# Performance work log

Measured on AMD Instinct MI355X. Metric: run time of the kernel, lower is better.

Reference implementation:

```python
import jax, jax.numpy as jnp
import numpy as np

B, HH, WW, D, NH, DK, DV, RATIO = 16, 48, 48, 512, 8, 64, 64, 3
EPS = 1e-5

def setup_inputs() -> dict:
    key = jax.random.key(0)
    ks = jax.random.split(key, 12)
    nq = HH * WW
    w = lambda i, shape: jax.random.normal(ks[i], shape, jnp.float32) * 0.02
    return {
        "queries": jax.random.normal(ks[0], (B, nq, D), jnp.float32),
        "Wq": w(1, (D, NH * DK)), "bq": jnp.zeros((NH * DK,), jnp.float32),
        "Wk": w(2, (D, NH * DK)), "bk": jnp.zeros((NH * DK,), jnp.float32),
        "Wv": w(3, (D, NH * DV)), "bv": jnp.zeros((NH * DV,), jnp.float32),
        "Wo": w(4, (NH * DV, D)), "bo": jnp.zeros((D,), jnp.float32),
        "sr_w": w(5, (D, 1, RATIO + 1, RATIO + 1)),  # depthwise conv, OIHW with I=1
        "sr_b": jnp.zeros((D,), jnp.float32),
        "ln_g": jnp.ones((D,), jnp.float32), "ln_b": jnp.zeros((D,), jnp.float32),
        "tw": w(6, (NH, NH)),  # 1x1 conv over head dim
        "tb": jnp.zeros((NH,), jnp.float32),
    }


def reference(queries, Wq, bq, Wk, bk, Wv, bv, Wo, bo, sr_w, sr_b, ln_g, ln_b, tw, tb):
    b, nq, c = queries.shape
    # Q projection -> (b, h, nq, d_k)
    q = (queries @ Wq + bq).reshape(b, nq, NH, DK).transpose(0, 2, 1, 3)
    # spatial reduction: depthwise strided conv over (H, W)
    x = queries.transpose(0, 2, 1).reshape(b, c, HH, WW)
    pad = RATIO // 2
    x = jax.lax.conv_general_dilated(
        x, sr_w, window_strides=(RATIO, RATIO),
        padding=[(pad, pad), (pad, pad)], feature_group_count=c,
        dimension_numbers=("NCHW", "OIHW", "NCHW"))
    x = x + sr_b[None, :, None, None]
    nk = x.shape[2] * x.shape[3]
    x = x.reshape(b, c, nk).transpose(0, 2, 1)  # (b, nk, c)
    # LayerNorm over channel dim
    mu = x.mean(-1, keepdims=True)
    var = x.var(-1, keepdims=True)
    x = (x - mu) / jnp.sqrt(var + EPS) * ln_g + ln_b
    # K, V projections
    k = (x @ Wk + bk).reshape(b, nk, NH, DK).transpose(0, 2, 3, 1)  # (b,h,d_k,nk)
    v = (x @ Wv + bv).reshape(b, nk, NH, DV).transpose(0, 2, 1, 3)  # (b,h,nk,d_v)
    # scaled attention scores
    att = jnp.einsum("bhqd,bhdk->bhqk", q, k) / jnp.sqrt(jnp.float32(DK))
    # transform: 1x1 conv over heads -> softmax(-1) -> InstanceNorm2d (no affine)
    att = jnp.einsum("oi,biqk->boqk", tw, att) + tb[None, :, None, None]
    att = jax.nn.softmax(att, axis=-1)
    m = att.mean((2, 3), keepdims=True)
    va = att.var((2, 3), keepdims=True)
    att = (att - m) / jnp.sqrt(va + EPS)
    # apply to values and output projection
    out = jnp.einsum("bhqk,bhkd->bhqd", att, v).transpose(0, 2, 1, 3).reshape(b, nq, NH * DV)
    return out @ Wo + bo
```

## Files before the change

kernel.cpp:

```cpp
#include <hip/hip_runtime.h>
#include <hip/hip_bf16.h>
#include <stdint.h>


typedef __bf16 bf16;
typedef __bf16 bf16x4 __attribute__((ext_vector_type(4)));
typedef __bf16 bf16x8 __attribute__((ext_vector_type(8)));
typedef float  f32x4  __attribute__((ext_vector_type(4)));

#define LDS_AS  __attribute__((address_space(3)))
#define GLOB_AS __attribute__((address_space(1)))

__device__ __forceinline__ void gload_lds16(const bf16* g, void* l) {
    __builtin_amdgcn_global_load_lds((const GLOB_AS void*)g, (LDS_AS void*)l, 16, 0, 0);
}

#define NB   16
#define NQ   2304
#define DD   512
#define NKV  256

constexpr size_t OFF_WQT = 0;
constexpr size_t OFF_WKT = 512*512*2;
constexpr size_t OFF_WVT = 2*512*512*2;
constexpr size_t OFF_WOT = 3*512*512*2;
constexpr size_t OFF_X   = 4*512*512*2;
constexpr size_t OFF_KT  = OFF_X  + 4194304;
constexpr size_t OFF_VT  = OFF_KT + 4194304;
constexpr size_t OFF_SS  = OFF_VT + 4194304;
constexpr size_t OFF_SM  = OFF_SS + 512;
constexpr size_t OFF_TWF = OFF_SM + 40192;
constexpr size_t OFF_FLG = OFF_TWF + 256;
constexpr size_t OFF_QF  = OFF_FLG + 256;
constexpr size_t OFF_U   = OFF_QF + (size_t)NB*NQ*DD*2;
constexpr size_t OFF_S   = OFF_U  + (size_t)NB*NQ*DD*2;
constexpr size_t SPLANE  = (size_t)NQ*NKV*2;
constexpr size_t OFF_WOTP = OFF_X;

#define SM_BQ   0
#define SM_BK   512
#define SM_BV   1024
#define SM_BO   1536
#define SM_SRW  2048
#define SM_SRB  10240
#define SM_LNG  10752
#define SM_LNB  11264
#define SM_TW   11776
#define SM_SRWT 11840

__global__ __launch_bounds__(64) void detect_dtype(const uint32_t* __restrict__ q,
                                                   int* __restrict__ flag)
{
    int t = threadIdx.x;
    int cnt = 0;
    #pragma unroll
    for (int i = 0; i < 8; i++) {
        uint32_t w = q[t*8 + i];
        int e = (w >> 7) & 0xFF;
        cnt += (e >= 100 && e <= 150) ? 1 : 0;
    }
    #pragma unroll
    for (int m = 1; m < 64; m <<= 1) cnt += __shfl_xor(cnt, m);
    if (t == 0) *flag = (cnt >= 384) ? 0 : 1;
}

__global__ __launch_bounds__(256) void convert_q(const void* __restrict__ in,
                                                 bf16* __restrict__ out,
                                                 const int* __restrict__ flag)
{
    if (*flag == 0) return;
    int idx = blockIdx.x * 256 + threadIdx.x;
    f32x4 a = ((const f32x4*)in)[(size_t)idx*2];
    f32x4 b = ((const f32x4*)in)[(size_t)idx*2 + 1];
    bf16x8 r;
    #pragma unroll
    for (int i = 0; i < 4; i++) { r[i] = (bf16)a[i]; r[i+4] = (bf16)b[i]; }
    ((bf16x8*)out)[idx] = r;
}

__global__ __launch_bounds__(256) void convert_small(
    const void* s0, const void* s1, const void* s2, const void* s3,
    const void* s4, const void* s5, const void* s6, const void* s7,
    const void* s8, bf16* __restrict__ dst, float* __restrict__ twf,
    const int* __restrict__ flag)
{
    const void* srcs[9] = {s0,s1,s2,s3,s4,s5,s6,s7,s8};
    const int sizes[9]  = {512,512,512,512,8192,512,512,512,64};
    const int offs[9]   = {SM_BQ,SM_BK,SM_BV,SM_BO,SM_SRW,SM_SRB,SM_LNG,SM_LNB,SM_TW};
    const float scl[9]  = {0.125f,1.f,1.f,1.f,1.f,1.f,1.f,1.f,1.f};
    int b = blockIdx.x;
    const void* s = srcs[b];
    int n = sizes[b], o = offs[b];
    float sc = scl[b];
    bool f32 = (*flag != 0);
    for (int i = threadIdx.x; i < n; i += 256) {
        float v = f32 ? ((const float*)s)[i] : (float)((const bf16*)s)[i];
        dst[o + i] = (bf16)(v * sc);
        if (b == 8) twf[i] = v;
        if (b == 4) {
            int tap = i & 15, ch = i >> 4;
            dst[SM_SRWT + tap*DD + ch] = (bf16)v;
        }
    }
}

__global__ __launch_bounds__(256) void transpose512(
    const void* s0, const void* s1, const void* s2, const void* s3,
    bf16* __restrict__ d0, bf16* __restrict__ d1,
    bf16* __restrict__ d2, bf16* __restrict__ d3,
    const int* __restrict__ flag)
{
    __shared__ bf16 tile[32][33];
    bool f32 = (*flag != 0);
    int wsel = blockIdx.z;
    const void* src = wsel == 0 ? s0 : wsel == 1 ? s1 : wsel == 2 ? s2 : s3;
    bf16*       dst = wsel == 0 ? d0 : wsel == 1 ? d1 : wsel == 2 ? d2 : d3;
    float scl = (wsel == 0) ? 0.125f : 1.0f;
    int c0 = blockIdx.x * 32, n0 = blockIdx.y * 32;
    int tx = threadIdx.x, ty = threadIdx.y;
    #pragma unroll
    for (int i = 0; i < 4; i++) {
        size_t idx = (size_t)(c0 + ty + i*8) * 512 + n0 + tx;
        float v = f32 ? ((const float*)src)[idx] : (float)((const bf16*)src)[idx];
        tile[ty + i*8][tx] = (bf16)(v * scl);
    }
    __syncthreads();
    #pragma unroll
    for (int i = 0; i < 4; i++)
        dst[(size_t)(n0 + ty + i*8) * 512 + c0 + tx] = tile[tx][ty + i*8];
}

__global__ __launch_bounds__(256) void sr_ln(
    const void* __restrict__ qraw, const bf16* __restrict__ qc,
    const bf16* __restrict__ sm, bf16* __restrict__ x,
    const int* __restrict__ flag)
{
    const bf16* q = (*flag) ? qc : (const bf16*)qraw;
    const int t = threadIdx.x;
    const int w = t >> 6, lane = t & 63;
    const int pos = blockIdx.x * 4 + w;
    const int b = pos >> 8, ok = pos & 255;
    const int oh = ok >> 4, ow = ok & 15;
    const int c0 = lane * 8;

    float acc[8] = {};
    #pragma unroll
    for (int kh = 0; kh < 4; kh++) {
        int ih = oh*3 - 1 + kh;
        if (ih < 0) continue;
        #pragma unroll
        for (int kw = 0; kw < 4; kw++) {
            int iw = ow*3 - 1 + kw;
            if (iw < 0) continue;
            bf16x8 qv = *(const bf16x8*)(q + ((size_t)b*NQ + ih*48 + iw)*DD + c0);
            bf16x8 wv = *(const bf16x8*)(sm + SM_SRWT + (kh*4 + kw)*DD + c0);
            #pragma unroll
            for (int r = 0; r < 8; r++) acc[r] += (float)qv[r] * (float)wv[r];
        }
    }
    bf16x8 sb = *(const bf16x8*)(sm + SM_SRB + c0);
    #pragma unroll
    for (int r = 0; r < 8; r++) acc[r] += (float)sb[r];

    float s = 0.f, s2 = 0.f;
    #pragma unroll
    for (int r = 0; r < 8; r++) { s += acc[r]; s2 += acc[r]*acc[r]; }
    #pragma unroll
    for (int m = 1; m < 64; m <<= 1) { s += __shfl_xor(s, m); s2 += __shfl_xor(s2, m); }
    float mu  = s * (1.f/512.f);
    float var = s2 * (1.f/512.f) - mu*mu;
    float inv = rsqrtf(var + 1e-5f);

    bf16x8 gv = *(const bf16x8*)(sm + SM_LNG + c0);
    bf16x8 bv = *(const bf16x8*)(sm + SM_LNB + c0);
    bf16x8 outv;
    #pragma unroll
    for (int r = 0; r < 8; r++)
        outv[r] = (bf16)((acc[r] - mu) * inv * (float)gv[r] + (float)bv[r]);
    *(bf16x8*)(x + (size_t)pos * DD + c0) = outv;
}

template <int MODE>
__global__ __launch_bounds__(256) void gemm_bt(
    const bf16* __restrict__ A, const bf16* __restrict__ Bt,
    const bf16* __restrict__ bias, bf16* __restrict__ C,
    const int* __restrict__ of32, const bf16* __restrict__ A2)
{
    constexpr int K = 512;
    __shared__ bf16 Al[128 * 64];
    __shared__ bf16 Bl[128 * 64];
    const int m0 = blockIdx.x * 128, n0 = blockIdx.y * 128;
    const int t = threadIdx.x;
    const int lane = t & 63, w = t >> 6;
    const int wr = w >> 1, wc = w & 1;
    const int gg = lane >> 4, li = lane & 15;
    const int fsw = (li & 7) << 4;
    bool f32o = false;
    if (MODE == 2) f32o = (*of32 != 0);

    const bf16* Ab = A;
    if (MODE == 4) Ab = (*of32) ? A2 : A;
    const bf16* Btb = Bt;
    if (MODE == 2) Btb = Bt + (size_t)(m0 / 2304) * (512 * 512);

    f32x4 acc[4][4] = {};

    for (int k0 = 0; k0 < K; k0 += 64) {
        #pragma unroll
        for (int p = 0; p < 4; p++) {
            int off = p*4096 + t*16;
            int row = off >> 7;
            int col = ((((off >> 4) & 7) ^ (row & 7)) << 3);
            gload_lds16(Ab + (size_t)(m0 + row)*K + k0 + col, (char*)Al + off);
        }
        #pragma unroll
        for (int p = 0; p < 4; p++) {
            int off = p*4096 + t*16;
            int row = off >> 7;
            int col = ((((off >> 4) & 7) ^ (row & 7)) << 3);
            gload_lds16(Btb + (size_t)(n0 + row)*K + k0 + col, (char*)Bl + off);
        }
        __syncthreads();
        #pragma unroll
        for (int kk = 0; kk < 2; kk++) {
            bf16x8 af[4], bfr[4];
            #pragma unroll
            for (int i = 0; i < 4; i++) {
                af[i]  = *(const bf16x8*)((char*)Al + (wr*64 + i*16 + li)*128 + ((kk*64 + gg*16) ^ fsw));
                bfr[i] = *(const bf16x8*)((char*)Bl + (wc*64 + i*16 + li)*128 + ((kk*64 + gg*16) ^ fsw));
            }
            __builtin_amdgcn_s_setprio(1);
            #pragma unroll
            for (int i = 0; i < 4; i++)
                #pragma unroll
                for (int j = 0; j < 4; j++)
                    acc[i][j] = __builtin_amdgcn_mfma_f32_16x16x32_bf16(af[i], bfr[j], acc[i][j], 0, 0, 0);
            __builtin_amdgcn_s_setprio(0);
        }
        __syncthreads();
    }

    #pragma unroll
    for (int i = 0; i < 4; i++) {
        #pragma unroll
        for (int j = 0; j < 4; j++) {
            int rbase = m0 + wr*64 + i*16 + gg*4;
            int c     = n0 + wc*64 + j*16 + li;
            float bv = (float)bias[c];
            #pragma unroll
            for (int jj = 0; jj < 4; jj++) {
                float val = acc[i][j][jj] + bv;
                int r = rbase + jj;
                if (MODE == 1) {
                    int bb = r >> 8, kk2 = r & 255;
                    int hh = c >> 6, dv = c & 63;
                    C[(((size_t)(bb*8 + hh))*64 + dv)*256 + kk2] = (bf16)val;
                } else if (MODE == 2) {
                    if (f32o) ((float*)C)[(size_t)r * 512 + c] = val;
                    else      C[(size_t)r * 512 + c] = (bf16)val;
                } else {
                    C[(size_t)r * 512 + c] = (bf16)val;
                }
            }
        }
    }
}

__global__ __launch_bounds__(256) void gemm_s(
    const bf16* __restrict__ Qf, const bf16* __restrict__ Kt, bf16* __restrict__ S,
    int b0)
{
    __shared__ bf16 Al[128 * 64];
    __shared__ bf16 Bl[128 * 64];
    const int m0 = blockIdx.x * 128, n0 = blockIdx.y * 128;
    const int bo = blockIdx.z;
    const int b = b0 + (bo >> 3), ih = bo & 7;
    const int t = threadIdx.x;
    const int lane = t & 63, w = t >> 6;
    const int wr = w >> 1, wc = w & 1;
    const int gg = lane >> 4, li = lane & 15;
    const int fsw = (li & 7) << 4;

    #pragma unroll
    for (int p = 0; p < 4; p++) {
        int off = p*4096 + t*16;
        int row = off >> 7;
        int col = ((((off >> 4) & 7) ^ (row & 7)) << 3);
        gload_lds16(Qf + ((size_t)(b*NQ + m0 + row))*DD + ih*64 + col, (char*)Al + off);
    }
    #pragma unroll
    for (int p = 0; p < 4; p++) {
        int off = p*4096 + t*16;
        int row = off >> 7;
        int col = ((((off >> 4) & 7) ^ (row & 7)) << 3);
        gload_lds16(Kt + ((size_t)(b*NKV + n0 + row))*DD + ih*64 + col, (char*)Bl + off);
    }
    __syncthreads();

    f32x4 acc[4][4] = {};
    #pragma unroll
    for (int kk = 0; kk < 2; kk++) {
        bf16x8 af[4], bfr[4];
        #pragma unroll
        for (int i = 0; i < 4; i++) {
            af[i]  = *(const bf16x8*)((char*)Al + (wr*64 + i*16 + li)*128 + ((kk*64 + gg*16) ^ fsw));
            bfr[i] = *(const bf16x8*)((char*)Bl + (wc*64 + i*16 + li)*128 + ((kk*64 + gg*16) ^ fsw));
        }
        __builtin_amdgcn_s_setprio(1);
        #pragma unroll
        for (int i = 0; i < 4; i++)
            #pragma unroll
            for (int j = 0; j < 4; j++)
                acc[i][j] = __builtin_amdgcn_mfma_f32_16x16x32_bf16(af[i], bfr[j], acc[i][j], 0, 0, 0);
        __builtin_amdgcn_s_setprio(0);
    }

    bf16* Sb = S + (size_t)bo * NQ * NKV;
    #pragma unroll
    for (int i = 0; i < 4; i++) {
        #pragma unroll
        for (int j = 0; j < 4; j++) {
            int rbase = m0 + wr*64 + i*16 + gg*4;
            int c     = n0 + wc*64 + j*16 + li;
            #pragma unroll
            for (int jj = 0; jj < 4; jj++)
                Sb[(size_t)(rbase + jj) * NKV + c] = (bf16)acc[i][j][jj];
        }
    }
}

__global__ __launch_bounds__(256) void mix_softmax(
    bf16* __restrict__ S, const float* __restrict__ twf,
    float* __restrict__ ssq_g, int b0)
{
    const int t = threadIdx.x;
    const int lane = t & 63, w = t >> 6;
    const int bl = blockIdx.y;
    const int b  = b0 + bl;
    const int q0 = blockIdx.x * 32 + w * 8;
    __shared__ float rpar[4][8];

    float tw[8][8];
    #pragma unroll
    for (int o = 0; o < 8; o++)
        #pragma unroll
        for (int i = 0; i < 8; i++)
            tw[o][i] = twf[o*8 + i];

    float ssqL[8] = {};
    for (int qi = 0; qi < 8; qi++) {
        float s[8][4];
        #pragma unroll
        for (int i = 0; i < 8; i++) {
            bf16x4 v = *(const bf16x4*)(S + (((size_t)(bl*8 + i))*NQ + (q0 + qi))*NKV + lane*4);
            #pragma unroll
            for (int r = 0; r < 4; r++) s[i][r] = (float)v[r];
        }
        float e[8][4], inv[8];
        #pragma unroll
        for (int o = 0; o < 8; o++) {
            float sum = 0.f;
            #pragma unroll
            for (int r = 0; r < 4; r++) {
                float a = 0.f;
                #pragma unroll
                for (int i = 0; i < 8; i++) a += tw[o][i] * s[i][r];
                e[o][r] = __expf(a);
                sum += e[o][r];
            }
            #pragma unroll
            for (int m = 1; m < 64; m <<= 1) sum += __shfl_xor(sum, m);
            inv[o] = 1.0f / sum;
        }
        #pragma unroll
        for (int o = 0; o < 8; o++) {
            bf16x4 dv;
            #pragma unroll
            for (int r = 0; r < 4; r++) {
                float d = e[o][r] * inv[o] - (1.0f/256.0f);
                ssqL[o] += d * d;
                dv[r] = (bf16)d;
            }
            *(bf16x4*)(S + (((size_t)(bl*8 + o))*NQ + (q0 + qi))*NKV + lane*4) = dv;
        }
    }
    #pragma unroll
    for (int o = 0; o < 8; o++) {
        float s = ssqL[o];
        #pragma unroll
        for (int m = 1; m < 64; m <<= 1) s += __shfl_xor(s, m);
        if (lane == 0) rpar[w][o] = s;
    }
    __syncthreads();
    if (t < 8) {
        float tot = rpar[0][t] + rpar[1][t] + rpar[2][t] + rpar[3][t];
        atomicAdd(&ssq_g[b*8 + t], tot);
    }
}

__global__ __launch_bounds__(256) void gemm_pv(
    const bf16* __restrict__ Dev, const bf16* __restrict__ VT, bf16* __restrict__ U,
    int b0)
{
    __shared__ bf16 Al[128 * 64];
    __shared__ bf16 Bl[64 * 64];
    const int m0 = blockIdx.x * 128;
    const int bo = blockIdx.y;
    const int b = b0 + (bo >> 3), o = bo & 7;
    const int t = threadIdx.x;
    const int lane = t & 63, w = t >> 6;
    const int wr = w >> 1, wc = w & 1;
    const int gg = lane >> 4, li = lane & 15;
    const int fsw = (li & 7) << 4;

    const bf16* Ab = Dev + (size_t)bo * NQ * NKV;
    const bf16* Bb = VT + ((size_t)(b*8 + o)) * 64 * NKV;

    f32x4 acc[4][2] = {};

    for (int k0 = 0; k0 < 256; k0 += 64) {
        #pragma unroll
        for (int p = 0; p < 4; p++) {
            int off = p*4096 + t*16;
            int row = off >> 7;
            int col = ((((off >> 4) & 7) ^ (row & 7)) << 3);
            gload_lds16(Ab + (size_t)(m0 + row)*NKV + k0 + col, (char*)Al + off);
        }
        #pragma unroll
        for (int p = 0; p < 2; p++) {
            int off = p*4096 + t*16;
            int row = off >> 7;
            int col = ((((off >> 4) & 7) ^ (row & 7)) << 3);
            gload_lds16(Bb + (size_t)row*NKV + k0 + col, (char*)Bl + off);
        }
        __syncthreads();
        #pragma unroll
        for (int kk = 0; kk < 2; kk++) {
            bf16x8 af[4], bfr[2];
            #pragma unroll
            for (int i = 0; i < 4; i++)
                af[i] = *(const bf16x8*)((char*)Al + (wr*64 + i*16 + li)*128 + ((kk*64 + gg*16) ^ fsw));
            #pragma unroll
            for (int j = 0; j < 2; j++)
                bfr[j] = *(const bf16x8*)((char*)Bl + (wc*32 + j*16 + li)*128 + ((kk*64 + gg*16) ^ fsw));
            __builtin_amdgcn_s_setprio(1);
            #pragma unroll
            for (int i = 0; i < 4; i++)
                #pragma unroll
                for (int j = 0; j < 2; j++)
                    acc[i][j] = __builtin_amdgcn_mfma_f32_16x16x32_bf16(af[i], bfr[j], acc[i][j], 0, 0, 0);
            __builtin_amdgcn_s_setprio(0);
        }
        __syncthreads();
    }

    #pragma unroll
    for (int i = 0; i < 4; i++) {
        #pragma unroll
        for (int j = 0; j < 2; j++) {
            int rbase = m0 + wr*64 + i*16 + gg*4;
            int c = wc*32 + j*16 + li;
            #pragma unroll
            for (int jj = 0; jj < 4; jj++)
                U[((size_t)b*NQ + rbase + jj)*DD + o*64 + c] = (bf16)acc[i][j][jj];
        }
    }
}

__global__ __launch_bounds__(256) void scale_wot(const bf16* __restrict__ WoT,
                                                 const float* __restrict__ ssq,
                                                 bf16* __restrict__ out)
{
    int idx = blockIdx.x * 256 + threadIdx.x;
    int c8 = idx & 63;
    int c  = (idx >> 6) & 511;
    int b  = idx >> 15;
    int h  = c8 >> 3;
    float va = ssq[b*8 + h] * (1.0f / ((float)NQ * (float)NKV));
    float s  = rsqrtf(va + 1e-5f);
    bf16x8 v = *(const bf16x8*)(WoT + ((size_t)c << 9) + c8*8);
    bf16x8 r;
    #pragma unroll
    for (int i = 0; i < 8; i++) r[i] = (bf16)((float)v[i] * s);
    *(bf16x8*)(out + ((size_t)idx << 3)) = r;
}

extern "C" void kernel_launch(void* const* d_in, const int* in_sizes, int n_in,
                              void* d_out, int out_size, void* d_ws, size_t ws_size,
                              hipStream_t stream)
{
    const void* queries = d_in[0];
    const void* Wq = d_in[1];  const void* bq = d_in[2];
    const void* Wk = d_in[3];  const void* bk = d_in[4];
    const void* Wv = d_in[5];  const void* bv = d_in[6];
    const void* Wo = d_in[7];  const void* bo = d_in[8];
    const void* srw = d_in[9]; const void* srb = d_in[10];
    const void* lng = d_in[11]; const void* lnb = d_in[12];
    const void* tw  = d_in[13];

    char* ws = (char*)d_ws;
    bf16* WqT = (bf16*)(ws + OFF_WQT);
    bf16* WkT = (bf16*)(ws + OFF_WKT);
    bf16* WvT = (bf16*)(ws + OFF_WVT);
    bf16* WoT = (bf16*)(ws + OFF_WOT);
    bf16* xb  = (bf16*)(ws + OFF_X);
    bf16* Kt  = (bf16*)(ws + OFF_KT);
    bf16* VTb = (bf16*)(ws + OFF_VT);
    bf16* Qf  = (bf16*)(ws + OFF_QF);
    bf16* Ub  = (bf16*)(ws + OFF_U);
    float* ss = (float*)(ws + OFF_SS);
    bf16* sm  = (bf16*)(ws + OFF_SM);
    float* twf = (float*)(ws + OFF_TWF);
    int* flag = (int*)(ws + OFF_FLG);
    bf16* WoTp = (bf16*)(ws + OFF_WOTP);
    bf16* Sb  = (bf16*)(ws + OFF_S);
    bf16* Qc  = Ub;

    int CB = 1;
    if      (OFF_S + 8*8*SPLANE <= ws_size) CB = 8;
    else if (OFF_S + 4*8*SPLANE <= ws_size) CB = 4;
    else if (OFF_S + 2*8*SPLANE <= ws_size) CB = 2;

    detect_dtype<<<dim3(1), dim3(64), 0, stream>>>((const uint32_t*)queries, flag);
    hipMemsetAsync(ss, 0, 128 * sizeof(float), stream);

    convert_q<<<dim3(9216), dim3(256), 0, stream>>>(queries, Qc, flag);
    convert_small<<<dim3(9), dim3(256), 0, stream>>>(bq, bk, bv, bo, srw, srb, lng, lnb, tw, sm, twf, flag);
    transpose512<<<dim3(16, 16, 4), dim3(32, 8), 0, stream>>>(Wq, Wk, Wv, Wo, WqT, WkT, WvT, WoT, flag);

    sr_ln<<<dim3(NB * NKV / 4), dim3(256), 0, stream>>>(queries, Qc, sm, xb, flag);
    gemm_bt<0><<<dim3(32, 4), dim3(256), 0, stream>>>(xb, WkT, sm + SM_BK, Kt, nullptr, nullptr);
    gemm_bt<1><<<dim3(32, 4), dim3(256), 0, stream>>>(xb, WvT, sm + SM_BV, VTb, nullptr, nullptr);
    gemm_bt<4><<<dim3(288, 4), dim3(256), 0, stream>>>((const bf16*)queries, WqT, sm + SM_BQ, Qf, flag, Qc);

    for (int b0 = 0; b0 < NB; b0 += CB) {
        gemm_s<<<dim3(18, 2, CB*8), dim3(256), 0, stream>>>(Qf, Kt, Sb, b0);
        mix_softmax<<<dim3(72, CB), dim3(256), 0, stream>>>(Sb, twf, ss, b0);
        gemm_pv<<<dim3(18, CB*8), dim3(256), 0, stream>>>(Sb, VTb, Ub, b0);
    }

    scale_wot<<<dim3(2048), dim3(256), 0, stream>>>(WoT, ss, WoTp);
    gemm_bt<2><<<dim3(288, 4), dim3(256), 0, stream>>>(Ub, WoTp, sm + SM_BO, (bf16*)d_out, flag, nullptr);
}
```

Before: 329.6 us.

## Fuse QK^T, head-mix softmax and PV into one LDS-resident attention kernel

Replaces the three-kernel attention loop (score GEMM, head-mixing softmax, PV GEMM) with one kernel. Each block handles 16 queries across all 8 heads and keeps the score tile in LDS, so the large score tensor never goes to global memory. The old kernels wrote and read that tensor several times, and this removes that traffic and the batch-chunked launch loop. In exchange, K and V fragments are loaded straight from global memory without LDS staging, and each block does little MFMA work. K/V are reloaded by every query block, though L2 should mostly absorb that.

```diff
diff --git a/kernel.cpp b/kernel.cpp
--- a/kernel.cpp
+++ b/kernel.cpp
@@ -33,8 +33,6 @@
 constexpr size_t OFF_FLG = OFF_TWF + 256;
 constexpr size_t OFF_QF  = OFF_FLG + 256;
 constexpr size_t OFF_U   = OFF_QF + (size_t)NB*NQ*DD*2;
-constexpr size_t OFF_S   = OFF_U  + (size_t)NB*NQ*DD*2;
-constexpr size_t SPLANE  = (size_t)NQ*NKV*2;
 constexpr size_t OFF_WOTP = OFF_X;
 
 #define SM_BQ   0
@@ -266,79 +264,38 @@
     }
 }
 
-__global__ __launch_bounds__(256) void gemm_s(
-    const bf16* __restrict__ Qf, const bf16* __restrict__ Kt, bf16* __restrict__ S,
-    int b0)
-{
-    __shared__ bf16 Al[128 * 64];
-    __shared__ bf16 Bl[128 * 64];
-    const int m0 = blockIdx.x * 128, n0 = blockIdx.y * 128;
-    const int bo = blockIdx.z;
-    const int b = b0 + (bo >> 3), ih = bo & 7;
+__global__ __launch_bounds__(512, 4) void attn_lds(
+    const bf16* __restrict__ Qf, const bf16* __restrict__ Kt,
+    const bf16* __restrict__ VT, const float* __restrict__ twf,
+    bf16* __restrict__ U, float* __restrict__ ssq_g)
+{
+    __shared__ bf16 Sl[8][16][264];
+    __shared__ float rpar[8][8];
+
     const int t = threadIdx.x;
     const int lane = t & 63, w = t >> 6;
-    const int wr = w >> 1, wc = w & 1;
     const int gg = lane >> 4, li = lane & 15;
-    const int fsw = (li & 7) << 4;
-
-    #pragma unroll
-    for (int p = 0; p < 4; p++) {
-        int off = p*4096 + t*16;
-        int row = off >> 7;
-        int col = ((((off >> 4) & 7) ^ (row & 7)) << 3);
-        gload_lds16(Qf + ((size_t)(b*NQ + m0 + row))*DD + ih*64 + col, (char*)Al + off);
-    }
-    #pragma unroll
-    for (int p = 0; p < 4; p++) {
-        int off = p*4096 + t*16;
-        int row = off >> 7;
-        int col = ((((off >> 4) & 7) ^ (row & 7)) << 3);
-        gload_lds16(Kt + ((size_t)(b*NKV + n0 + row))*DD + ih*64 + col, (char*)Bl + off);
+    const int b = blockIdx.y;
+    const int q0 = blockIdx.x * 16;
+
+    {
+        const bf16* Qb = Qf + ((size_t)(b*NQ + q0 + li))*DD + w*64 + gg*8;
+        const bf16* Kb = Kt + ((size_t)(b*NKV + li))*DD + w*64 + gg*8;
+        bf16x8 af0 = *(const bf16x8*)(Qb);
+        bf16x8 af1 = *(const bf16x8*)(Qb + 32);
+        #pragma unroll
+        for (int nt = 0; nt < 16; nt++) {
+            bf16x8 b0 = *(const bf16x8*)(Kb + (size_t)(nt*16)*DD);
+            bf16x8 b1 = *(const bf16x8*)(Kb + (size_t)(nt*16)*DD + 32);
+            f32x4 a = {};
+            a = __builtin_amdgcn_mfma_f32_16x16x32_bf16(af0, b0, a, 0, 0, 0);
+            a = __builtin_amdgcn_mfma_f32_16x16x32_bf16(af1, b1, a, 0, 0, 0);
+            #pragma unroll
+            for (int jj = 0; jj < 4; jj++)
+                Sl[w][gg*4 + jj][nt*16 + li] = (bf16)a[jj];
+        }
     }
     __syncthreads();
-
-    f32x4 acc[4][4] = {};
-    #pragma unroll
-    for (int kk = 0; kk < 2; kk++) {
-        bf16x8 af[4], bfr[4];
-        #pragma unroll
-        for (int i = 0; i < 4; i++) {
-            af[i]  = *(const bf16x8*)((char*)Al + (wr*64 + i*16 + li)*128 + ((kk*64 + gg*16) ^ fsw));
-            bfr[i] = *(const bf16x8*)((char*)Bl + (wc*64 + i*16 + li)*128 + ((kk*64 + gg*16) ^ fsw));
-        }
-        __builtin_amdgcn_s_setprio(1);
-        #pragma unroll
-        for (int i = 0; i < 4; i++)
-            #pragma unroll
-            for (int j = 0; j < 4; j++)
-                acc[i][j] = __builtin_amdgcn_mfma_f32_16x16x32_bf16(af[i], bfr[j], acc[i][j], 0, 0, 0);
-        __builtin_amdgcn_s_setprio(0);
-    }
-
-    bf16* Sb = S + (size_t)bo * NQ * NKV;
-    #pragma unroll
-    for (int i = 0; i < 4; i++) {
-        #pragma unroll
-        for (int j = 0; j < 4; j++) {
-            int rbase = m0 + wr*64 + i*16 + gg*4;
-            int c     = n0 + wc*64 + j*16 + li;
-            #pragma unroll
-            for (int jj = 0; jj < 4; jj++)
-                Sb[(size_t)(rbase + jj) * NKV + c] = (bf16)acc[i][j][jj];
-        }
-    }
-}
-
-__global__ __launch_bounds__(256) void mix_softmax(
-    bf16* __restrict__ S, const float* __restrict__ twf,
-    float* __restrict__ ssq_g, int b0)
-{
-    const int t = threadIdx.x;
-    const int lane = t & 63, w = t >> 6;
-    const int bl = blockIdx.y;
-    const int b  = b0 + bl;
-    const int q0 = blockIdx.x * 32 + w * 8;
-    __shared__ float rpar[4][8];
 
     float tw[8][8];
     #pragma unroll
@@ -348,11 +305,13 @@
             tw[o][i] = twf[o*8 + i];
 
     float ssqL[8] = {};
-    for (int qi = 0; qi < 8; qi++) {
+    #pragma unroll
+    for (int qi = 0; qi < 2; qi++) {
+        const int q = w*2 + qi;
         float s[8][4];
         #pragma unroll
         for (int i = 0; i < 8; i++) {
-            bf16x4 v = *(const bf16x4*)(S + (((size_t)(bl*8 + i))*NQ + (q0 + qi))*NKV + lane*4);
+            bf16x4 v = *(const bf16x4*)&Sl[i][q][lane*4];
             #pragma unroll
             for (int r = 0; r < 4; r++) s[i][r] = (float)v[r];
         }
@@ -381,7 +340,7 @@
                 ssqL[o] += d * d;
                 dv[r] = (bf16)d;
             }
-            *(bf16x4*)(S + (((size_t)(bl*8 + o))*NQ + (q0 + qi))*NKV + lane*4) = dv;
+            *(bf16x4*)&Sl[o][q][lane*4] = dv;
         }
     }
     #pragma unroll
@@ -393,76 +352,34 @@
     }
     __syncthreads();
     if (t < 8) {
-        float tot = rpar[0][t] + rpar[1][t] + rpar[2][t] + rpar[3][t];
+        float tot = 0.f;
+        #pragma unroll
+        for (int i = 0; i < 8; i++) tot += rpar[i][t];
         atomicAdd(&ssq_g[b*8 + t], tot);
     }
-}
-
-__global__ __launch_bounds__(256) void gemm_pv(
-    const bf16* __restrict__ Dev, const bf16* __restrict__ VT, bf16* __restrict__ U,
-    int b0)
-{
-    __shared__ bf16 Al[128 * 64];
-    __shared__ bf16 Bl[64 * 64];
-    const int m0 = blockIdx.x * 128;
-    const int bo = blockIdx.y;
-    const int b = b0 + (bo >> 3), o = bo & 7;
-    const int t = threadIdx.x;
-    const int lane = t & 63, w = t >> 6;
-    const int wr = w >> 1, wc = w & 1;
-    const int gg = lane >> 4, li = lane & 15;
-    const int fsw = (li & 7) << 4;
-
-    const bf16* Ab = Dev + (size_t)bo * NQ * NKV;
-    const bf16* Bb = VT + ((size_t)(b*8 + o)) * 64 * NKV;
-
-    f32x4 acc[4][2] = {};
-
-    for (int k0 = 0; k0 < 256; k0 += 64) {
-        #pragma unroll
-        for (int p = 0; p < 4; p++) {
-            int off = p*4096 + t*16;
-            int row = off >> 7;
-            int col = ((((off >> 4) & 7) ^ (row & 7)) << 3);
-            gload_lds16(Ab + (size_t)(m0 + row)*NKV + k0 + col, (char*)Al + off);
-        }
-        #pragma unroll
-        for (int p = 0; p < 2; p++) {
-            int off = p*4096 + t*16;
-            int row = off >> 7;
-            int col = ((((off >> 4) & 7) ^ (row & 7)) << 3);
-            gload_lds16(Bb + (size_t)row*NKV + k0 + col, (char*)Bl + off);
-        }
-        __syncthreads();
-        #pragma unroll
-        for (int kk = 0; kk < 2; kk++) {
-            bf16x8 af[4], bfr[2];
-            #pragma unroll
-            for (int i = 0; i < 4; i++)
-                af[i] = *(const bf16x8*)((char*)Al + (wr*64 + i*16 + li)*128 + ((kk*64 + gg*16) ^ fsw));
-            #pragma unroll
-            for (int j = 0; j < 2; j++)
-                bfr[j] = *(const bf16x8*)((char*)Bl + (wc*32 + j*16 + li)*128 + ((kk*64 + gg*16) ^ fsw));
-            __builtin_amdgcn_s_setprio(1);
-            #pragma unroll
-            for (int i = 0; i < 4; i++)
-                #pragma unroll
-                for (int j = 0; j < 2; j++)
-                    acc[i][j] = __builtin_amdgcn_mfma_f32_16x16x32_bf16(af[i], bfr[j], acc[i][j], 0, 0, 0);
-            __builtin_amdgcn_s_setprio(0);
-        }
-        __syncthreads();
-    }
-
-    #pragma unroll
-    for (int i = 0; i < 4; i++) {
-        #pragma unroll
-        for (int j = 0; j < 2; j++) {
-            int rbase = m0 + wr*64 + i*16 + gg*4;
-            int c = wc*32 + j*16 + li;
-            #pragma unroll
-            for (int jj = 0; jj < 4; jj++)
-                U[((size_t)b*NQ + rbase + jj)*DD + o*64 + c] = (bf16)acc[i][j][jj];
+
+    {
+        const bf16* Vb = VT + ((size_t)(b*8 + w))*64*NKV + (size_t)li*NKV + gg*8;
+        f32x4 u0 = {}, u1 = {}, u2 = {}, u3 = {};
+        #pragma unroll
+        for (int ks = 0; ks < 8; ks++) {
+            bf16x8 af = *(const bf16x8*)&Sl[w][li][ks*32 + gg*8];
+            bf16x8 b0 = *(const bf16x8*)(Vb + ks*32);
+            u0 = __builtin_amdgcn_mfma_f32_16x16x32_bf16(af, b0, u0, 0, 0, 0);
+            bf16x8 b1 = *(const bf16x8*)(Vb + (size_t)16*NKV + ks*32);
+            u1 = __builtin_amdgcn_mfma_f32_16x16x32_bf16(af, b1, u1, 0, 0, 0);
+            bf16x8 b2 = *(const bf16x8*)(Vb + (size_t)32*NKV + ks*32);
+            u2 = __builtin_amdgcn_mfma_f32_16x16x32_bf16(af, b2, u2, 0, 0, 0);
+            bf16x8 b3 = *(const bf16x8*)(Vb + (size_t)48*NKV + ks*32);
+            u3 = __builtin_amdgcn_mfma_f32_16x16x32_bf16(af, b3, u3, 0, 0, 0);
+        }
+        #pragma unroll
+        for (int jj = 0; jj < 4; jj++) {
+            bf16* row = U + ((size_t)(b*NQ + q0 + gg*4 + jj))*DD + w*64 + li;
+            row[0]  = (bf16)u0[jj];
+            row[16] = (bf16)u1[jj];
+            row[32] = (bf16)u2[jj];
+            row[48] = (bf16)u3[jj];
         }
     }
 }
@@ -513,13 +430,7 @@
     float* twf = (float*)(ws + OFF_TWF);
     int* flag = (int*)(ws + OFF_FLG);
     bf16* WoTp = (bf16*)(ws + OFF_WOTP);
-    bf16* Sb  = (bf16*)(ws + OFF_S);
     bf16* Qc  = Ub;
-
-    int CB = 1;
-    if      (OFF_S + 8*8*SPLANE <= ws_size) CB = 8;
-    else if (OFF_S + 4*8*SPLANE <= ws_size) CB = 4;
-    else if (OFF_S + 2*8*SPLANE <= ws_size) CB = 2;
 
     detect_dtype<<<dim3(1), dim3(64), 0, stream>>>((const uint32_t*)queries, flag);
     hipMemsetAsync(ss, 0, 128 * sizeof(float), stream);
@@ -533,11 +444,7 @@
     gemm_bt<1><<<dim3(32, 4), dim3(256), 0, stream>>>(xb, WvT, sm + SM_BV, VTb, nullptr, nullptr);
     gemm_bt<4><<<dim3(288, 4), dim3(256), 0, stream>>>((const bf16*)queries, WqT, sm + SM_BQ, Qf, flag, Qc);
 
-    for (int b0 = 0; b0 < NB; b0 += CB) {
-        gemm_s<<<dim3(18, 2, CB*8), dim3(256), 0, stream>>>(Qf, Kt, Sb, b0);
-        mix_softmax<<<dim3(72, CB), dim3(256), 0, stream>>>(Sb, twf, ss, b0);
-        gemm_pv<<<dim3(18, CB*8), dim3(256), 0, stream>>>(Sb, VTb, Ub, b0);
-    }
+    attn_lds<<<dim3(144, 16), dim3(512), 0, stream>>>(Qf, Kt, VTb, twf, Ub, ss);
 
     scale_wot<<<dim3(2048), dim3(256), 0, stream>>>(WoT, ss, WoTp);
     gemm_bt<2><<<dim3(288, 4), dim3(256), 0, stream>>>(Ub, WoTp, sm + SM_BO, (bf16*)d_out, flag, nullptr);
```

New measurement: 313.2 us. -5.0%, faster.
